# Kernel tuning notes

Measured on AMD Instinct MI355X. Metric: run time of the kernel, lower is better.

Reference implementation:

```python
import jax, jax.numpy as jnp
import numpy as np

B, L, DIM = 2, 2048, 1024
DI = 2 * DIM          # d_inner (expand=2)
DS = 16               # d_state
DTR = DIM // 16       # dt_rank
K = 4                 # conv kernel size


def setup_inputs() -> dict:
    key = jax.random.key(0)
    ks = jax.random.split(key, 9)
    def rn(k, shape, scale):
        return jax.random.normal(k, shape, dtype=jnp.float32) * scale
    # S4D-real init for A
    A_log = jnp.log(jnp.broadcast_to(jnp.arange(1, DS + 1, dtype=jnp.float32), (DI, DS)))
    return dict(
        x=rn(ks[0], (B, L, DIM), 1.0),
        W_in=rn(ks[1], (DIM, 2 * DI), 0.02),
        conv_w=rn(ks[2], (DI, 1, K), 0.1),   # depthwise conv kernel [out_ch, in_ch/groups, K]
        conv_b=rn(ks[3], (DI,), 0.02),
        W_xproj=rn(ks[4], (DI, DTR + 2 * DS), 0.02),
        W_dt=rn(ks[5], (DTR, DI), 0.05),
        b_dt=rn(ks[6], (DI,), 0.5),
        A_log=A_log,
        D=jnp.ones((DI,), jnp.float32),
        W_out=rn(ks[7], (DI, DIM), 0.02),
    )


def reference(x, W_in, conv_w, conv_b, W_xproj, W_dt, b_dt, A_log, D, W_out):
    # x: [B, L, DIM]
    xz = x @ W_in                                  # [B, L, 2*DI]
    xp, z = jnp.split(xz, 2, axis=-1)              # each [B, L, DI]

    # Causal depthwise conv1d along L
    xc = jnp.transpose(xp, (0, 2, 1))              # [B, DI, L]
    xc = jax.lax.conv_general_dilated(
        xc, conv_w, window_strides=(1,), padding=[(K - 1, 0)],
        feature_group_count=DI)
    xc = xc + conv_b[None, :, None]
    xp = jax.nn.silu(jnp.transpose(xc, (0, 2, 1)))  # [B, L, DI]

    # Input-dependent dt, B, C
    dbl = xp @ W_xproj                              # [B, L, DTR + 2*DS]
    dt, Bm, Cm = jnp.split(dbl, [DTR, DTR + DS], axis=-1)
    dt = jax.nn.softplus(dt @ W_dt + b_dt)          # [B, L, DI]

    A = -jnp.exp(A_log)                             # [DI, DS]

    def step(h, t):
        dt_t, B_t, C_t, x_t = t                     # [B,DI], [B,DS], [B,DS], [B,DI]
        dA = jnp.exp(dt_t[..., None] * A)           # [B, DI, DS]
        h = dA * h + dt_t[..., None] * B_t[:, None, :] * x_t[..., None]
        y = jnp.einsum('bds,bs->bd', h, C_t)        # [B, DI]
        return h, y

    h0 = jnp.zeros((B, DI, DS), x.dtype)
    ts = (dt.transpose(1, 0, 2), Bm.transpose(1, 0, 2),
          Cm.transpose(1, 0, 2), xp.transpose(1, 0, 2))
    _, ys = jax.lax.scan(step, h0, ts)              # ys: [L, B, DI]
    y = ys.transpose(1, 0, 2) + xp * D              # skip connection
    y = y * jax.nn.silu(z)                          # gate
    return y @ W_out                                # [B, L, DIM]
```

## Files before the change

kernel.cpp:

```cpp
#include <hip/hip_runtime.h>
#include <cstdint>
#include <cstddef>

#define CB   2
#define CL   2048
#define CDIM 1024
#define CDI  2048
#define CDS  16
#define CDTR 64
#define NCHUNK 16
#define CHLEN  (CL / NCHUNK)
#define TSTEP  32

enum { EPI_ATOMIC_N96 = 1, EPI_SOFTPLUS = 2 };

typedef __attribute__((ext_vector_type(8))) short bf16x8;
typedef __attribute__((ext_vector_type(4))) float f32x4;

#define AS1 __attribute__((address_space(1)))
#define AS3 __attribute__((address_space(3)))

__device__ __forceinline__ void gld16(const void* g, void* l) {
    __builtin_amdgcn_global_load_lds((const AS1 unsigned int*)g,
                                     (AS3 unsigned int*)l, 16, 0, 0);
}

__device__ __forceinline__ float sigmoidf_fast(float x) {
    return 1.0f / (1.0f + __expf(-x));
}
__device__ __forceinline__ unsigned short f2bf(float f) {
    unsigned int u = __float_as_uint(f);
    u = u + 0x7fffu + ((u >> 16) & 1u);
    return (unsigned short)(u >> 16);
}
__device__ __forceinline__ float bf2f(unsigned short h) {
    return __uint_as_float(((unsigned int)h) << 16);
}

__global__ __launch_bounds__(256) void gemm_bf16x3(
    const unsigned short* __restrict__ Ah, const unsigned short* __restrict__ Al,
    const unsigned short* __restrict__ Bh, const unsigned short* __restrict__ Bl,
    float* __restrict__ C, int N, int K, int nbx, int nwg)
{
    __shared__ unsigned short sm[16384];
    char* smB = (char*)sm;

    const int bid = blockIdx.x;
    const int q = nwg >> 3, r = nwg & 7;
    const int xcd = bid & 7, idx = bid >> 3;
    const int wg = (xcd < r ? xcd * (q + 1) : r * (q + 1) + (xcd - r) * q) + idx;
    const int bx = wg % nbx, by = wg / nbx;
    const int m0 = by << 7, n0 = bx << 7;

    const int tid = threadIdx.x;
    const int wid = tid >> 6, lane = tid & 63;

    unsigned int rS[2], cS[2];
    #pragma unroll
    for (int iss = 0; iss < 2; ++iss) {
        unsigned int X = iss * 4096u + (unsigned int)tid * 16u;
        rS[iss] = X >> 6;
        cS[iss] = (X & 63u) >> 1;
    }
    const unsigned short* pAh = Ah + (size_t)m0 * K;
    const unsigned short* pAl = Al + (size_t)m0 * K;
    const unsigned short* pBh = Bh + (size_t)n0 * K;
    const unsigned short* pBl = Bl + (size_t)n0 * K;

    const int fr = lane & 15, kg = lane >> 4;
    const int wr = (wid >> 1) << 6, wc = (wid & 1) << 6;
    unsigned int offA[4], offB[4];
    #pragma unroll
    for (int i = 0; i < 4; ++i) {
        offA[i] = (unsigned int)(wr + i * 16 + fr) * 64u + (unsigned int)kg * 16u;
        offB[i] = (unsigned int)(wc + i * 16 + fr) * 64u + (unsigned int)kg * 16u;
    }

    f32x4 acc[4][4];
    #pragma unroll
    for (int i = 0; i < 4; ++i)
        #pragma unroll
        for (int j = 0; j < 4; ++j)
            acc[i][j] = (f32x4){0.f, 0.f, 0.f, 0.f};

    for (int kt = 0; kt < K; kt += 32) {
        __syncthreads();
        #pragma unroll
        for (int iss = 0; iss < 2; ++iss) {
            char* l = smB + iss * 4096 + wid * 1024;
            const size_t ro = (size_t)rS[iss] * K + cS[iss] + kt;
            gld16(pAh + ro, l);
            gld16(pAl + ro, l + 8192);
            gld16(pBh + ro, l + 16384);
            gld16(pBl + ro, l + 24576);
        }
        __syncthreads();

        bf16x8 ah[4], al4[4], bh[4], bl4[4];
        #pragma unroll
        for (int i = 0; i < 4; ++i) {
            ah[i]  = *(const bf16x8*)(smB + offA[i]);
            al4[i] = *(const bf16x8*)(smB + 8192 + offA[i]);
            bh[i]  = *(const bf16x8*)(smB + 16384 + offB[i]);
            bl4[i] = *(const bf16x8*)(smB + 24576 + offB[i]);
        }
        #pragma unroll
        for (int i = 0; i < 4; ++i)
            #pragma unroll
            for (int j = 0; j < 4; ++j) {
                acc[i][j] = __builtin_amdgcn_mfma_f32_16x16x32_bf16(ah[i],  bh[j],  acc[i][j], 0, 0, 0);
                acc[i][j] = __builtin_amdgcn_mfma_f32_16x16x32_bf16(ah[i],  bl4[j], acc[i][j], 0, 0, 0);
                acc[i][j] = __builtin_amdgcn_mfma_f32_16x16x32_bf16(al4[i], bh[j],  acc[i][j], 0, 0, 0);
            }
    }

    #pragma unroll
    for (int i = 0; i < 4; ++i) {
        const int rrb = m0 + wr + i * 16 + kg * 4;
        #pragma unroll
        for (int j = 0; j < 4; ++j) {
            const int cc = n0 + wc + j * 16 + fr;
            #pragma unroll
            for (int v = 0; v < 4; ++v)
                C[(size_t)(rrb + v) * N + cc] = acc[i][j][v];
        }
    }
}

__global__ __launch_bounds__(256) void cvt_split(
    const float* __restrict__ in, unsigned short* __restrict__ hi,
    unsigned short* __restrict__ lo, int n4)
{
    const int i = blockIdx.x * 256 + threadIdx.x;
    if (i >= n4) return;
    const float4 v = ((const float4*)in)[i];
    ushort4 h, l;
    h.x = f2bf(v.x); l.x = f2bf(v.x - bf2f(h.x));
    h.y = f2bf(v.y); l.y = f2bf(v.y - bf2f(h.y));
    h.z = f2bf(v.z); l.z = f2bf(v.z - bf2f(h.z));
    h.w = f2bf(v.w); l.w = f2bf(v.w - bf2f(h.w));
    ((ushort4*)hi)[i] = h;
    ((ushort4*)lo)[i] = l;
}

__global__ __launch_bounds__(256) void cvt_split_T(
    const float* __restrict__ W, int K, int N,
    unsigned short* __restrict__ Th, unsigned short* __restrict__ Tl)
{
    __shared__ float t[64][65];
    const int n0 = blockIdx.x * 64, k0 = blockIdx.y * 64;
    const int tid = threadIdx.x;
    const int c4 = (tid & 15) << 2;
    const int r  = tid >> 4;
    #pragma unroll
    for (int p = 0; p < 4; ++p) {
        const int k = r + p * 16;
        const float4 v = *(const float4*)&W[(size_t)(k0 + k) * N + n0 + c4];
        t[c4 + 0][k] = v.x; t[c4 + 1][k] = v.y;
        t[c4 + 2][k] = v.z; t[c4 + 3][k] = v.w;
    }
    __syncthreads();
    #pragma unroll
    for (int p = 0; p < 4; ++p) {
        const int n = r + p * 16;
        const float a = t[n][c4], b = t[n][c4 + 1], c = t[n][c4 + 2], d = t[n][c4 + 3];
        ushort4 h, l;
        h.x = f2bf(a); l.x = f2bf(a - bf2f(h.x));
        h.y = f2bf(b); l.y = f2bf(b - bf2f(h.y));
        h.z = f2bf(c); l.z = f2bf(c - bf2f(h.z));
        h.w = f2bf(d); l.w = f2bf(d - bf2f(h.w));
        *(ushort4*)&Th[(size_t)(n0 + n) * K + k0 + c4] = h;
        *(ushort4*)&Tl[(size_t)(n0 + n) * K + k0 + c4] = l;
    }
}

template<int EPI>
__global__ __launch_bounds__(256) void sgemm128(
    const float* __restrict__ A, int lda,
    const float* __restrict__ Bm, int ldb,
    float* __restrict__ C, int ldc,
    int KB, const float* __restrict__ bias)
{
    __shared__ float As[8][128];
    __shared__ float Bs[8][128];
    const int tid = threadIdx.x;
    const int m0 = blockIdx.y * 128;
    const int n0 = blockIdx.x * 128;
    const int k0 = blockIdx.z * KB;

    const int aRow = tid >> 1;
    const int aCol = (tid & 1) << 2;
    const int bRow = tid >> 5;
    const int bCol = (tid & 31) << 2;
    const int tr = tid >> 4;
    const int tc = tid & 15;

    const float* Ap = A + (size_t)(m0 + aRow) * lda + k0 + aCol;
    const float* Bp = Bm + (size_t)(k0 + bRow) * ldb + n0 + bCol;

    float4 aReg = *(const float4*)Ap;
    float4 bReg;
    if (EPI == EPI_ATOMIC_N96 && (n0 + bCol) >= 96)
        bReg = make_float4(0.f, 0.f, 0.f, 0.f);
    else
        bReg = *(const float4*)Bp;

    float acc[8][8];
    #pragma unroll
    for (int i = 0; i < 8; ++i)
        #pragma unroll
        for (int j = 0; j < 8; ++j) acc[i][j] = 0.0f;

    const int nIter = KB >> 3;
    for (int kt = 0; kt < nIter; ++kt) {
        __syncthreads();
        As[aCol + 0][aRow] = aReg.x;
        As[aCol + 1][aRow] = aReg.y;
        As[aCol + 2][aRow] = aReg.z;
        As[aCol + 3][aRow] = aReg.w;
        *(float4*)&Bs[bRow][bCol] = bReg;
        __syncthreads();
        if (kt + 1 < nIter) {
            aReg = *(const float4*)(Ap + (size_t)(kt + 1) * 8);
            const float* bp2 = Bp + (size_t)(kt + 1) * 8 * ldb;
            if (EPI == EPI_ATOMIC_N96 && (n0 + bCol) >= 96)
                bReg = make_float4(0.f, 0.f, 0.f, 0.f);
            else
                bReg = *(const float4*)bp2;
        }
        #pragma unroll
        for (int k = 0; k < 8; ++k) {
            const float4 a0 = *(const float4*)&As[k][(tr << 2)];
            const float4 a1 = *(const float4*)&As[k][64 + (tr << 2)];
            const float4 b0 = *(const float4*)&Bs[k][(tc << 2)];
            const float4 b1 = *(const float4*)&Bs[k][64 + (tc << 2)];
            const float af[8] = {a0.x, a0.y, a0.z, a0.w, a1.x, a1.y, a1.z, a1.w};
            const float bf[8] = {b0.x, b0.y, b0.z, b0.w, b1.x, b1.y, b1.z, b1.w};
            #pragma unroll
            for (int i = 0; i < 8; ++i)
                #pragma unroll
                for (int j = 0; j < 8; ++j)
                    acc[i][j] = fmaf(af[i], bf[j], acc[i][j]);
        }
    }

    #pragma unroll
    for (int i = 0; i < 8; ++i) {
        const int m = m0 + ((i < 4) ? ((tr << 2) + i) : (64 + (tr << 2) + (i - 4)));
        if (EPI == EPI_SOFTPLUS) {
            float v[8];
            #pragma unroll
            for (int j = 0; j < 8; ++j) {
                const int n = (j < 4) ? (n0 + (tc << 2) + j) : (n0 + 64 + (tc << 2) + (j - 4));
                float t = acc[i][j] + bias[n];
                v[j] = fmaxf(t, 0.0f) + log1pf(__expf(-fabsf(t)));
            }
            *(float4*)&C[(size_t)m * ldc + n0 + (tc << 2)]      = make_float4(v[0], v[1], v[2], v[3]);
            *(float4*)&C[(size_t)m * ldc + n0 + 64 + (tc << 2)] = make_float4(v[4], v[5], v[6], v[7]);
        } else {
            #pragma unroll
            for (int j = 0; j < 8; ++j) {
                const int n = (j < 4) ? ((tc << 2) + j) : (64 + (tc << 2) + (j - 4));
                if (n < 96) atomicAdd(&C[(size_t)m * 96 + n], acc[i][j]);
            }
        }
    }
}

__global__ __launch_bounds__(256) void conv_silu_k(
    const float* __restrict__ xz, const float* __restrict__ cw,
    const float* __restrict__ cb, float* __restrict__ xp)
{
    const int idx = blockIdx.x * 256 + threadIdx.x;
    const int d4 = (idx & 511) << 2;
    const int t  = (idx >> 9) & 2047;
    const int b  = idx >> 20;
    const size_t rb = (size_t)(b * CL + t) * 4096 + d4;
    float4 acc = *(const float4*)&cb[d4];
    const float4 w0 = *(const float4*)&cw[(d4 + 0) << 2];
    const float4 w1 = *(const float4*)&cw[(d4 + 1) << 2];
    const float4 w2 = *(const float4*)&cw[(d4 + 2) << 2];
    const float4 w3 = *(const float4*)&cw[(d4 + 3) << 2];
    float4 xv;
    if (t >= 3) {
        xv = *(const float4*)&xz[rb - 3 * 4096];
        acc.x = fmaf(w0.x, xv.x, acc.x); acc.y = fmaf(w1.x, xv.y, acc.y);
        acc.z = fmaf(w2.x, xv.z, acc.z); acc.w = fmaf(w3.x, xv.w, acc.w);
    }
    if (t >= 2) {
        xv = *(const float4*)&xz[rb - 2 * 4096];
        acc.x = fmaf(w0.y, xv.x, acc.x); acc.y = fmaf(w1.y, xv.y, acc.y);
        acc.z = fmaf(w2.y, xv.z, acc.z); acc.w = fmaf(w3.y, xv.w, acc.w);
    }
    if (t >= 1) {
        xv = *(const float4*)&xz[rb - 1 * 4096];
        acc.x = fmaf(w0.z, xv.x, acc.x); acc.y = fmaf(w1.z, xv.y, acc.y);
        acc.z = fmaf(w2.z, xv.z, acc.z); acc.w = fmaf(w3.z, xv.w, acc.w);
    }
    {
        xv = *(const float4*)&xz[rb];
        acc.x = fmaf(w0.w, xv.x, acc.x); acc.y = fmaf(w1.w, xv.y, acc.y);
        acc.z = fmaf(w2.w, xv.z, acc.z); acc.w = fmaf(w3.w, xv.w, acc.w);
    }
    acc.x *= sigmoidf_fast(acc.x);
    acc.y *= sigmoidf_fast(acc.y);
    acc.z *= sigmoidf_fast(acc.z);
    acc.w *= sigmoidf_fast(acc.w);
    *(float4*)&xp[(size_t)(b * CL + t) * 2048 + d4] = acc;
}

__global__ __launch_bounds__(256) void zero_f4(float4* __restrict__ p, int n4)
{
    const int i = blockIdx.x * 256 + threadIdx.x;
    if (i < n4) p[i] = make_float4(0.f, 0.f, 0.f, 0.f);
}


__global__ __launch_bounds__(256) void scan_part1(
    const float* __restrict__ dt, const float* __restrict__ xp,
    const float* __restrict__ dbl, const float* __restrict__ A_log,
    float* __restrict__ Pc, float* __restrict__ Hc)
{
    __shared__ float dtS[TSTEP][64];
    __shared__ float xS [TSTEP][64];
    __shared__ float BS [TSTEP][16];

    const int tid = threadIdx.x;
    const int bx  = blockIdx.x;
    const int ch  = blockIdx.y;
    const int b   = bx >> 5;
    const int d0  = (bx & 31) << 6;
    const int dloc = tid >> 2;
    const int s4   = tid & 3;
    const int d  = d0 + dloc;
    const int sg = s4 << 2;

    float Al2[4];
    #pragma unroll
    for (int j = 0; j < 4; ++j)
        Al2[j] = -__expf(A_log[d * CDS + sg + j]) * 1.44269504f;

    const int lr = tid >> 3;
    const int lc = (tid & 7) << 3;
    const int br = (tid & 127) >> 2;
    const int bc = (tid & 3) << 2;
    const int rbase = b * CL + ch * CHLEN;

    float4 rDt0, rDt1, rX0, rX1, rB;
    {
        const size_t row = (size_t)(rbase + lr) * 2048 + d0 + lc;
        rDt0 = *(const float4*)&dt[row];     rDt1 = *(const float4*)&dt[row + 4];
        rX0  = *(const float4*)&xp[row];     rX1  = *(const float4*)&xp[row + 4];
        if (tid < 128)
            rB = *(const float4*)&dbl[(size_t)(rbase + br) * 96 + 64 + bc];
    }

    float h[4] = {0.f, 0.f, 0.f, 0.f};
    float sdt = 0.f;

    #pragma unroll
    for (int tile = 0; tile < CHLEN / TSTEP; ++tile) {
        __syncthreads();
        *(float4*)&dtS[lr][lc] = rDt0;  *(float4*)&dtS[lr][lc + 4] = rDt1;
        *(float4*)&xS [lr][lc] = rX0;   *(float4*)&xS [lr][lc + 4] = rX1;
        if (tid < 128) *(float4*)&BS[br][bc] = rB;
        if (tile + 1 < CHLEN / TSTEP) {
            const size_t row = (size_t)(rbase + (tile + 1) * TSTEP + lr) * 2048 + d0 + lc;
            rDt0 = *(const float4*)&dt[row];  rDt1 = *(const float4*)&dt[row + 4];
            rX0  = *(const float4*)&xp[row];  rX1  = *(const float4*)&xp[row + 4];
            if (tid < 128)
                rB = *(const float4*)&dbl[(size_t)(rbase + (tile + 1) * TSTEP + br) * 96 + 64 + bc];
        }
        __syncthreads();
        #pragma unroll 4
        for (int tt = 0; tt < TSTEP; ++tt) {
            const float dtt = dtS[tt][dloc];
            const float xt  = xS [tt][dloc];
            const float4 Bv = *(const float4*)&BS[tt][sg];
            const float dtx = dtt * xt;
            sdt += dtt;
            h[0] = fmaf(exp2f(dtt * Al2[0]), h[0], dtx * Bv.x);
            h[1] = fmaf(exp2f(dtt * Al2[1]), h[1], dtx * Bv.y);
            h[2] = fmaf(exp2f(dtt * Al2[2]), h[2], dtx * Bv.z);
            h[3] = fmaf(exp2f(dtt * Al2[3]), h[3], dtx * Bv.w);
        }
    }

    #pragma unroll
    for (int j = 0; j < 4; ++j) {
        const int idx = ((b * CDI + d) * CDS + sg + j) * NCHUNK + ch;
        Pc[idx] = exp2f(Al2[j] * sdt);
        Hc[idx] = h[j];
    }
}

__global__ __launch_bounds__(256) void scan_combine(
    const float* __restrict__ Pc, const float* __restrict__ Hc,
    float* __restrict__ Hi)
{
    const int i = blockIdx.x * 256 + threadIdx.x;
    const float4* p4 = (const float4*)&Pc[(size_t)i * NCHUNK];
    const float4* h4 = (const float4*)&Hc[(size_t)i * NCHUNK];
    float4* o4 = (float4*)&Hi[(size_t)i * NCHUNK];
    float h = 0.0f;
    #pragma unroll
    for (int c = 0; c < NCHUNK / 4; ++c) {
        const float4 pc = p4[c];
        const float4 hc = h4[c];
        float4 o;
        o.x = h; h = fmaf(pc.x, h, hc.x);
        o.y = h; h = fmaf(pc.y, h, hc.y);
        o.z = h; h = fmaf(pc.z, h, hc.z);
        o.w = h; h = fmaf(pc.w, h, hc.w);
        o4[c] = o;
    }
}

__global__ __launch_bounds__(256) void scan_part2(
    const float* __restrict__ dt, const float* __restrict__ xp,
    const float* __restrict__ xz, const float* __restrict__ dbl,
    const float* __restrict__ A_log, const float* __restrict__ Dv,
    const float* __restrict__ Hi,
    unsigned short* __restrict__ ygh, unsigned short* __restrict__ ygl)
{
    __shared__ float dtS[TSTEP][64];
    __shared__ float xS [TSTEP][64];
    __shared__ float zS [TSTEP][64];
    __shared__ float BS [TSTEP][16];
    __shared__ float CS [TSTEP][16];
    __shared__ float yS [TSTEP][64];

    const int tid = threadIdx.x;
    const int bx  = blockIdx.x;
    const int ch  = blockIdx.y;
    const int b   = bx >> 5;
    const int d0  = (bx & 31) << 6;
    const int dloc = tid >> 2;
    const int s4   = tid & 3;
    const int d  = d0 + dloc;
    const int sg = s4 << 2;

    float Al2[4];
    #pragma unroll
    for (int j = 0; j < 4; ++j)
        Al2[j] = -__expf(A_log[d * CDS + sg + j]) * 1.44269504f;
    const float Dd = Dv[d];

    const int lr = tid >> 3;
    const int lc = (tid & 7) << 3;
    const int br = (tid & 127) >> 2;
    const int bc = (tid & 3) << 2;
    const bool isB = tid < 128;
    const int rbase = b * CL + ch * CHLEN;

    float4 rDt0, rDt1, rX0, rX1, rZ0, rZ1, rBC;
    {
        const size_t row = (size_t)(rbase + lr);
        rDt0 = *(const float4*)&dt[row * 2048 + d0 + lc];
        rDt1 = *(const float4*)&dt[row * 2048 + d0 + lc + 4];
        rX0  = *(const float4*)&xp[row * 2048 + d0 + lc];
        rX1  = *(const float4*)&xp[row * 2048 + d0 + lc + 4];
        rZ0  = *(const float4*)&xz[row * 4096 + 2048 + d0 + lc];
        rZ1  = *(const float4*)&xz[row * 4096 + 2048 + d0 + lc + 4];
        rBC  = *(const float4*)&dbl[(size_t)(rbase + br) * 96 + (isB ? 64 : 80) + bc];
    }

    float h[4];
    #pragma unroll
    for (int j = 0; j < 4; ++j)
        h[j] = Hi[((b * CDI + d) * CDS + sg + j) * NCHUNK + ch];

    #pragma unroll
    for (int tile = 0; tile < CHLEN / TSTEP; ++tile) {
        __syncthreads();
        *(float4*)&dtS[lr][lc] = rDt0;  *(float4*)&dtS[lr][lc + 4] = rDt1;
        *(float4*)&xS [lr][lc] = rX0;   *(float4*)&xS [lr][lc + 4] = rX1;
        *(float4*)&zS [lr][lc] = rZ0;   *(float4*)&zS [lr][lc + 4] = rZ1;
        if (isB) *(float4*)&BS[br][bc] = rBC; else *(float4*)&CS[br][bc] = rBC;
        if (tile + 1 < CHLEN / TSTEP) {
            const size_t row = (size_t)(rbase + (tile + 1) * TSTEP + lr);
            rDt0 = *(const float4*)&dt[row * 2048 + d0 + lc];
            rDt1 = *(const float4*)&dt[row * 2048 + d0 + lc + 4];
            rX0  = *(const float4*)&xp[row * 2048 + d0 + lc];
            rX1  = *(const float4*)&xp[row * 2048 + d0 + lc + 4];
            rZ0  = *(const float4*)&xz[row * 4096 + 2048 + d0 + lc];
            rZ1  = *(const float4*)&xz[row * 4096 + 2048 + d0 + lc + 4];
            rBC  = *(const float4*)&dbl[(size_t)(rbase + (tile + 1) * TSTEP + br) * 96 + (isB ? 64 : 80) + bc];
        }
        __syncthreads();
        #pragma unroll 4
        for (int tt = 0; tt < TSTEP; ++tt) {
            const float dtt = dtS[tt][dloc];
            const float xt  = xS [tt][dloc];
            const float4 Bv = *(const float4*)&BS[tt][sg];
            const float4 Cv = *(const float4*)&CS[tt][sg];
            const float dtx = dtt * xt;
            h[0] = fmaf(exp2f(dtt * Al2[0]), h[0], dtx * Bv.x);
            h[1] = fmaf(exp2f(dtt * Al2[1]), h[1], dtx * Bv.y);
            h[2] = fmaf(exp2f(dtt * Al2[2]), h[2], dtx * Bv.z);
            h[3] = fmaf(exp2f(dtt * Al2[3]), h[3], dtx * Bv.w);
            float p = h[0] * Cv.x;
            p = fmaf(h[1], Cv.y, p);
            p = fmaf(h[2], Cv.z, p);
            p = fmaf(h[3], Cv.w, p);
            p += __shfl_xor(p, 1);
            p += __shfl_xor(p, 2);
            if (s4 == 0) {
                const float zt = zS[tt][dloc];
                const float y = p + xt * Dd;
                yS[tt][dloc] = y * zt * sigmoidf_fast(zt);
            }
        }
        __syncthreads();
        {
            const size_t row = (size_t)(rbase + tile * TSTEP + lr) * 2048 + d0 + lc;
            const float4 v0 = *(const float4*)&yS[lr][lc];
            const float4 v1 = *(const float4*)&yS[lr][lc + 4];
            ushort4 h0, l0, h1, l1;
            h0.x = f2bf(v0.x); l0.x = f2bf(v0.x - bf2f(h0.x));
            h0.y = f2bf(v0.y); l0.y = f2bf(v0.y - bf2f(h0.y));
            h0.z = f2bf(v0.z); l0.z = f2bf(v0.z - bf2f(h0.z));
            h0.w = f2bf(v0.w); l0.w = f2bf(v0.w - bf2f(h0.w));
            h1.x = f2bf(v1.x); l1.x = f2bf(v1.x - bf2f(h1.x));
            h1.y = f2bf(v1.y); l1.y = f2bf(v1.y - bf2f(h1.y));
            h1.z = f2bf(v1.z); l1.z = f2bf(v1.z - bf2f(h1.z));
            h1.w = f2bf(v1.w); l1.w = f2bf(v1.w - bf2f(h1.w));
            *(ushort4*)&ygh[row]     = h0;  *(ushort4*)&ygh[row + 4] = h1;
            *(ushort4*)&ygl[row]     = l0;  *(ushort4*)&ygl[row + 4] = l1;
        }
    }
}

extern "C" void kernel_launch(void* const* d_in, const int* in_sizes, int n_in,
                              void* d_out, int out_size, void* d_ws, size_t ws_size,
                              hipStream_t stream)
{
    const float* x      = (const float*)d_in[0];
    const float* W_in   = (const float*)d_in[1];
    const float* conv_w = (const float*)d_in[2];
    const float* conv_b = (const float*)d_in[3];
    const float* W_xp   = (const float*)d_in[4];
    const float* W_dt   = (const float*)d_in[5];
    const float* b_dt   = (const float*)d_in[6];
    const float* A_log  = (const float*)d_in[7];
    const float* Dv     = (const float*)d_in[8];
    const float* W_out  = (const float*)d_in[9];
    float* out = (float*)d_out;

    float* ws  = (float*)d_ws;
    float* xz  = ws;
    float* xp  = xz  + (size_t)4096 * 4096;
    float* dbl = xp  + (size_t)4096 * 2048;
    float* dtb = dbl + (size_t)4096 * 96;
    unsigned short* xhi  = (unsigned short*)dtb;
    unsigned short* xlo  = xhi + (size_t)4096 * 1024;
    unsigned short* woTh = (unsigned short*)dtb;
    unsigned short* woTl = woTh + (size_t)1024 * 2048;
    float* after_dtb = dtb + (size_t)4096 * 2048;
    unsigned short* ygh = (unsigned short*)after_dtb;
    unsigned short* ygl = ygh + (size_t)4096 * 2048;
    unsigned short* wiTh = ygh;
    unsigned short* wiTl = ygl;
    float* Pc = after_dtb + (size_t)4096 * 2048;
    float* Hc = Pc + (size_t)65536 * NCHUNK;
    float* Hi = Hc + (size_t)65536 * NCHUNK;

    cvt_split<<<4096, 256, 0, stream>>>(x, xhi, xlo, 1048576);
    cvt_split_T<<<dim3(64, 16), 256, 0, stream>>>(W_in, 1024, 4096, wiTh, wiTl);

    gemm_bf16x3<<<1024, 256, 0, stream>>>(xhi, xlo, wiTh, wiTl, xz,
                                          4096, 1024, 32, 1024);

    conv_silu_k<<<8192, 256, 0, stream>>>(xz, conv_w, conv_b, xp);

    zero_f4<<<384, 256, 0, stream>>>((float4*)dbl, 98304);
    sgemm128<EPI_ATOMIC_N96><<<dim3(1, 32, 16), 256, 0, stream>>>(
        xp, CDI, W_xp, 96, dbl, 96, 128, nullptr);

    sgemm128<EPI_SOFTPLUS><<<dim3(16, 32, 1), 256, 0, stream>>>(
        dbl, 96, W_dt, CDI, dtb, CDI, CDTR, b_dt);

    scan_part1<<<dim3(64, NCHUNK), 256, 0, stream>>>(dtb, xp, dbl, A_log, Pc, Hc);
    scan_combine<<<256, 256, 0, stream>>>(Pc, Hc, Hi);
    scan_part2<<<dim3(64, NCHUNK), 256, 0, stream>>>(
        dtb, xp, xz, dbl, A_log, Dv, Hi, ygh, ygl);

    cvt_split_T<<<dim3(16, 32), 256, 0, stream>>>(W_out, 2048, 1024, woTh, woTl);

    gemm_bf16x3<<<256, 256, 0, stream>>>(ygh, ygl, woTh, woTl, out,
                                         1024, 2048, 8, 256);
}
```

Before: 611.3 us.

## Swizzle LDS layout in bf16x3 GEMM and replace atomic split-K with partial-buffer reduce

The bf16x3 GEMM now XOR-swizzles the 16-byte chunk index by row bits, both when loading global memory into LDS and when reading fragments, to cut LDS bank conflicts. The split-K x_proj sgemm no longer zeroes the output and does atomicAdds. Each K-slice writes its own partial buffer, and a separate reduce kernel sums the 16 slices into dbl. This removes atomic contention and the zero pass, but adds an extra kernel and about 6 MB of partial-buffer traffic.

```diff
diff --git a/kernel.cpp b/kernel.cpp
--- a/kernel.cpp
+++ b/kernel.cpp
@@ -12,7 +12,7 @@
 #define CHLEN  (CL / NCHUNK)
 #define TSTEP  32
 
-enum { EPI_ATOMIC_N96 = 1, EPI_SOFTPLUS = 2 };
+enum { EPI_PART = 1, EPI_SOFTPLUS = 2 };
 
 typedef __attribute__((ext_vector_type(8))) short bf16x8;
 typedef __attribute__((ext_vector_type(4))) float f32x4;
@@ -59,8 +59,9 @@
     #pragma unroll
     for (int iss = 0; iss < 2; ++iss) {
         unsigned int X = iss * 4096u + (unsigned int)tid * 16u;
-        rS[iss] = X >> 6;
-        cS[iss] = (X & 63u) >> 1;
+        unsigned int P = X ^ (((X >> 7) & 3u) << 4);
+        rS[iss] = P >> 6;
+        cS[iss] = (P & 63u) >> 1;
     }
     const unsigned short* pAh = Ah + (size_t)m0 * K;
     const unsigned short* pAl = Al + (size_t)m0 * K;
@@ -72,8 +73,12 @@
     unsigned int offA[4], offB[4];
     #pragma unroll
     for (int i = 0; i < 4; ++i) {
-        offA[i] = (unsigned int)(wr + i * 16 + fr) * 64u + (unsigned int)kg * 16u;
-        offB[i] = (unsigned int)(wc + i * 16 + fr) * 64u + (unsigned int)kg * 16u;
+        int row = wr + i * 16 + fr;
+        unsigned int bb = ((unsigned int)row << 6) + ((unsigned int)kg << 4);
+        offA[i] = bb ^ ((((unsigned int)row >> 1) & 3u) << 4);
+        row = wc + i * 16 + fr;
+        bb = ((unsigned int)row << 6) + ((unsigned int)kg << 4);
+        offB[i] = bb ^ ((((unsigned int)row >> 1) & 3u) << 4);
     }
 
     f32x4 acc[4][4];
@@ -200,7 +205,7 @@
 
     float4 aReg = *(const float4*)Ap;
     float4 bReg;
-    if (EPI == EPI_ATOMIC_N96 && (n0 + bCol) >= 96)
+    if (EPI == EPI_PART && (n0 + bCol) >= 96)
         bReg = make_float4(0.f, 0.f, 0.f, 0.f);
     else
         bReg = *(const float4*)Bp;
@@ -223,7 +228,7 @@
         if (kt + 1 < nIter) {
             aReg = *(const float4*)(Ap + (size_t)(kt + 1) * 8);
             const float* bp2 = Bp + (size_t)(kt + 1) * 8 * ldb;
-            if (EPI == EPI_ATOMIC_N96 && (n0 + bCol) >= 96)
+            if (EPI == EPI_PART && (n0 + bCol) >= 96)
                 bReg = make_float4(0.f, 0.f, 0.f, 0.f);
             else
                 bReg = *(const float4*)bp2;
@@ -258,13 +263,27 @@
             *(float4*)&C[(size_t)m * ldc + n0 + (tc << 2)]      = make_float4(v[0], v[1], v[2], v[3]);
             *(float4*)&C[(size_t)m * ldc + n0 + 64 + (tc << 2)] = make_float4(v[4], v[5], v[6], v[7]);
         } else {
+            float* Cp = C + (size_t)blockIdx.z * 4096 * 96;
             #pragma unroll
             for (int j = 0; j < 8; ++j) {
                 const int n = (j < 4) ? ((tc << 2) + j) : (64 + (tc << 2) + (j - 4));
-                if (n < 96) atomicAdd(&C[(size_t)m * 96 + n], acc[i][j]);
+                if (n < 96) Cp[(size_t)m * 96 + n] = acc[i][j];
             }
         }
     }
+}
+
+__global__ __launch_bounds__(256) void reduce_part(
+    const float4* __restrict__ part, float4* __restrict__ out4)
+{
+    const int i = blockIdx.x * 256 + threadIdx.x;
+    float4 s = part[i];
+    #pragma unroll
+    for (int ks = 1; ks < 16; ++ks) {
+        const float4 v = part[(size_t)ks * 98304 + i];
+        s.x += v.x; s.y += v.y; s.z += v.z; s.w += v.w;
+    }
+    out4[i] = s;
 }
 
 __global__ __launch_bounds__(256) void conv_silu_k(
@@ -307,12 +326,6 @@
     acc.z *= sigmoidf_fast(acc.z);
     acc.w *= sigmoidf_fast(acc.w);
     *(float4*)&xp[(size_t)(b * CL + t) * 2048 + d4] = acc;
-}
-
-__global__ __launch_bounds__(256) void zero_f4(float4* __restrict__ p, int n4)
-{
-    const int i = blockIdx.x * 256 + threadIdx.x;
-    if (i < n4) p[i] = make_float4(0.f, 0.f, 0.f, 0.f);
 }
 
 
@@ -554,6 +567,7 @@
     float* dtb = dbl + (size_t)4096 * 96;
     unsigned short* xhi  = (unsigned short*)dtb;
     unsigned short* xlo  = xhi + (size_t)4096 * 1024;
+    float* part = dtb;
     unsigned short* woTh = (unsigned short*)dtb;
     unsigned short* woTl = woTh + (size_t)1024 * 2048;
     float* after_dtb = dtb + (size_t)4096 * 2048;
@@ -573,9 +587,9 @@
 
     conv_silu_k<<<8192, 256, 0, stream>>>(xz, conv_w, conv_b, xp);
 
-    zero_f4<<<384, 256, 0, stream>>>((float4*)dbl, 98304);
-    sgemm128<EPI_ATOMIC_N96><<<dim3(1, 32, 16), 256, 0, stream>>>(
-        xp, CDI, W_xp, 96, dbl, 96, 128, nullptr);
+    sgemm128<EPI_PART><<<dim3(1, 32, 16), 256, 0, stream>>>(
+        xp, CDI, W_xp, 96, part, 96, 128, nullptr);
+    reduce_part<<<384, 256, 0, stream>>>((const float4*)part, (float4*)dbl);
 
     sgemm128<EPI_SOFTPLUS><<<dim3(16, 32, 1), 256, 0, stream>>>(
         dbl, 96, W_dt, CDI, dtb, CDI, CDTR, b_dt);
```

After: 506.8 us. 1.21x faster.
